# Kernel tuning notes

Measured on AMD Instinct MI355X. Metric: run time of the kernel, lower is better.

Reference implementation:

```python
import jax, jax.numpy as jnp
import numpy as np

TAU = 0.07
EPS_NORM = 1e-12  # F.normalize eps
EPS_LOG = 1e-8

N, D = 16384, 128

def setup_inputs() -> dict:
    key = jax.random.key(0)
    k1, k2, k3, k4, k5 = jax.random.split(key, 5)
    return {
        'feats': jax.random.normal(k1, (N, D), dtype=jnp.float32),
        'times': jax.random.uniform(k2, (N,), dtype=jnp.float32),
        'events': jax.random.randint(k3, (N,), 0, 2, dtype=jnp.int32),
        'ipcw_weights': jax.random.uniform(k4, (N,), dtype=jnp.float32),
        'proto': jax.random.normal(k5, (D,), dtype=jnp.float32),
    }

def _l2_normalize(x, axis):
    n = jnp.sqrt(jnp.sum(x * x, axis=axis, keepdims=True))
    return x / jnp.maximum(n, EPS_NORM)

def reference(feats, times, events, ipcw_weights, proto):
    feats_n = _l2_normalize(feats, axis=1)          # [N, D]
    proto_n = _l2_normalize(proto, axis=0)          # [D]
    logits = (feats_n @ proto_n) / TAU              # [N]
    # riskmask[i, j] = 1 if times[j] >= times[i]
    riskmask = (times[None, :] >= times[:, None]).astype(jnp.float32)  # [N, N]
    exp_logits = jnp.exp(logits)[None, :] * riskmask                    # [N, N]
    denom = exp_logits.sum(axis=1)                                      # [N]
    log_denom = jnp.log(denom + EPS_LOG)
    ev = events.astype(jnp.float32)
    loss_vec = -(logits - log_denom) * ev * ipcw_weights
    normalizer = (ev * ipcw_weights).sum()
    return loss_vec.sum() / (normalizer + EPS_LOG)
```

## Files before the change

### kernel.cpp

```cpp
#include <hip/hip_runtime.h>
#include <math.h>

#define NROWS 16384
#define DDIM  128
#define JCHUNK 2048

__device__ __forceinline__ float wave_reduce_sum(float v) {
    #pragma unroll
    for (int m = 32; m >= 1; m >>= 1) v += __shfl_xor(v, m, 64);
    return v;
}


__global__ void k_zero(float* __restrict__ denom, float* __restrict__ acc) {
    int i = blockIdx.x * blockDim.x + threadIdx.x;
    if (i < NROWS) denom[i] = 0.0f;
    if (i < 3) acc[i] = 0.0f;
}

__global__ void k_proto_norm(const float* __restrict__ proto, float* __restrict__ ws_f) {
    int lane = threadIdx.x;
    float2 p = ((const float2*)proto)[lane];
    float s = p.x * p.x + p.y * p.y;
    s = wave_reduce_sum(s);
    if (lane == 0) ws_f[2] = 1.0f / fmaxf(sqrtf(s), 1e-12f);
}

__global__ __launch_bounds__(256) void k_logits(
    const float* __restrict__ feats, const float* __restrict__ proto,
    const float* __restrict__ times, const float* __restrict__ ws_f,
    float* __restrict__ logits, float* __restrict__ te)
{
    int wave = threadIdx.x >> 6, lane = threadIdx.x & 63;
    int row = blockIdx.x * 4 + wave;
    float2 f = ((const float2*)feats)[row * 64 + lane];
    float2 p = ((const float2*)proto)[lane];
    float d  = f.x * p.x + f.y * p.y;
    float n2 = f.x * f.x + f.y * f.y;
    d  = wave_reduce_sum(d);
    n2 = wave_reduce_sum(n2);
    if (lane == 0) {
        float sp    = ws_f[2];
        float invfn = 1.0f / fmaxf(sqrtf(n2), 1e-12f);
        float logit = (d * sp * invfn) / 0.07f;
        logits[row]     = logit;
        te[2 * row]     = times[row];
        te[2 * row + 1] = expf(logit);
    }
}

__global__ __launch_bounds__(256) void k_denom(
    const float* __restrict__ times, const float* __restrict__ te,
    float* __restrict__ denom)
{
    __shared__ float4 sh[JCHUNK / 2];
    int t = threadIdx.x;
    int i = blockIdx.x * 256 + t;
    const float4* src = (const float4*)(te + (size_t)blockIdx.y * JCHUNK * 2);
    #pragma unroll
    for (int k = 0; k < 4; ++k) sh[t + 256 * k] = src[t + 256 * k];
    __syncthreads();
    float ti  = times[i];
    float acc = 0.0f;
    #pragma unroll 8
    for (int jj = 0; jj < JCHUNK / 2; ++jj) {
        float4 v = sh[jj];
        acc += (v.x >= ti) ? v.y : 0.0f;
        acc += (v.z >= ti) ? v.w : 0.0f;
    }
    atomicAdd(&denom[i], acc);
}

__global__ __launch_bounds__(256) void k_loss(
    const float* __restrict__ logits, const float* __restrict__ denom,
    const int* __restrict__ events, const float* __restrict__ w,
    float* __restrict__ acc)
{
    int i = blockIdx.x * 256 + threadIdx.x;
    float ev = (float)events[i];
    float wv = ev * w[i];
    float l  = logits[i];
    float ld = logf(denom[i] + 1e-8f);
    float loss = -(l - ld) * wv;
    loss = wave_reduce_sum(loss);
    wv   = wave_reduce_sum(wv);
    __shared__ float s1[4], s2[4];
    int wave = threadIdx.x >> 6, lane = threadIdx.x & 63;
    if (lane == 0) { s1[wave] = loss; s2[wave] = wv; }
    __syncthreads();
    if (threadIdx.x == 0) {
        atomicAdd(&acc[0], s1[0] + s1[1] + s1[2] + s1[3]);
        atomicAdd(&acc[1], s2[0] + s2[1] + s2[2] + s2[3]);
    }
}

__global__ void k_final(const float* __restrict__ acc, float* __restrict__ out) {
    out[0] = acc[0] / (acc[1] + 1e-8f);
}

extern "C" void kernel_launch(void* const* d_in, const int* in_sizes, int n_in,
                              void* d_out, int out_size, void* d_ws, size_t ws_size,
                              hipStream_t stream) {
    const float* feats  = (const float*)d_in[0];
    const float* times  = (const float*)d_in[1];
    const int*   events = (const int*)d_in[2];
    const float* w      = (const float*)d_in[3];
    const float* proto  = (const float*)d_in[4];
    float* out  = (float*)d_out;
    float* ws_f = (float*)d_ws;

    float* acc    = ws_f;
    float* logits = ws_f + 256;
    float* denom  = ws_f + 256 + NROWS;
    float* te     = ws_f + 256 + 2 * NROWS;

    k_zero<<<(NROWS + 255) / 256, 256, 0, stream>>>(denom, acc);
    k_proto_norm<<<1, 64, 0, stream>>>(proto, ws_f);
    k_logits<<<NROWS / 4, 256, 0, stream>>>(feats, proto, times, ws_f, logits, te);
    k_denom<<<dim3(NROWS / 256, NROWS / JCHUNK), 256, 0, stream>>>(times, te, denom);
    k_loss<<<NROWS / 256, 256, 0, stream>>>(logits, denom, events, w, acc);
    k_final<<<1, 1, 0, stream>>>(acc, out);
}
```

Before: 99.42 us.

## Fuse small kernels and register-block the risk-set denominator over four rows

Drops the zeroing and prototype-norm kernels: the zeroing moves into k_logits and each wave recomputes the prototype norm. The loss and final division become one single-block kernel with no global atomics. k_denom now has each thread accumulate four rows per shared-memory load, which cuts LDS traffic per comparison. JCHUNK shrinks to 512, giving 16x32 = 512 blocks versus the previous 64x8 = 512. Launch count falls from six to three, at the cost of a serial single-block reduction and more atomics per row on denom.

```diff
diff --git a/kernel.cpp b/kernel.cpp
--- a/kernel.cpp
+++ b/kernel.cpp
@@ -3,7 +3,7 @@
 
 #define NROWS 16384
 #define DDIM  128
-#define JCHUNK 2048
+#define JCHUNK 512
 
 __device__ __forceinline__ float wave_reduce_sum(float v) {
     #pragma unroll
@@ -12,37 +12,27 @@
 }
 
 
-__global__ void k_zero(float* __restrict__ denom, float* __restrict__ acc) {
-    int i = blockIdx.x * blockDim.x + threadIdx.x;
-    if (i < NROWS) denom[i] = 0.0f;
-    if (i < 3) acc[i] = 0.0f;
-}
-
-__global__ void k_proto_norm(const float* __restrict__ proto, float* __restrict__ ws_f) {
-    int lane = threadIdx.x;
-    float2 p = ((const float2*)proto)[lane];
-    float s = p.x * p.x + p.y * p.y;
-    s = wave_reduce_sum(s);
-    if (lane == 0) ws_f[2] = 1.0f / fmaxf(sqrtf(s), 1e-12f);
-}
-
 __global__ __launch_bounds__(256) void k_logits(
     const float* __restrict__ feats, const float* __restrict__ proto,
-    const float* __restrict__ times, const float* __restrict__ ws_f,
-    float* __restrict__ logits, float* __restrict__ te)
+    const float* __restrict__ times,
+    float* __restrict__ logits, float* __restrict__ te,
+    float* __restrict__ denom)
 {
+    if (blockIdx.x < 64) denom[blockIdx.x * 256 + threadIdx.x] = 0.0f;
     int wave = threadIdx.x >> 6, lane = threadIdx.x & 63;
     int row = blockIdx.x * 4 + wave;
     float2 f = ((const float2*)feats)[row * 64 + lane];
     float2 p = ((const float2*)proto)[lane];
     float d  = f.x * p.x + f.y * p.y;
     float n2 = f.x * f.x + f.y * f.y;
+    float p2 = p.x * p.x + p.y * p.y;
     d  = wave_reduce_sum(d);
     n2 = wave_reduce_sum(n2);
+    p2 = wave_reduce_sum(p2);
     if (lane == 0) {
-        float sp    = ws_f[2];
+        float invpn = 1.0f / fmaxf(sqrtf(p2), 1e-12f);
         float invfn = 1.0f / fmaxf(sqrtf(n2), 1e-12f);
-        float logit = (d * sp * invfn) / 0.07f;
+        float logit = (d * invpn * invfn) / 0.07f;
         logits[row]     = logit;
         te[2 * row]     = times[row];
         te[2 * row + 1] = expf(logit);
@@ -55,47 +45,53 @@
 {
     __shared__ float4 sh[JCHUNK / 2];
     int t = threadIdx.x;
-    int i = blockIdx.x * 256 + t;
     const float4* src = (const float4*)(te + (size_t)blockIdx.y * JCHUNK * 2);
-    #pragma unroll
-    for (int k = 0; k < 4; ++k) sh[t + 256 * k] = src[t + 256 * k];
+    sh[t] = src[t];
+    int ibase = blockIdx.x * 1024 + t;
+    float ti0 = times[ibase];
+    float ti1 = times[ibase + 256];
+    float ti2 = times[ibase + 512];
+    float ti3 = times[ibase + 768];
     __syncthreads();
-    float ti  = times[i];
-    float acc = 0.0f;
-    #pragma unroll 8
+    float a0 = 0.f, a1 = 0.f, a2 = 0.f, a3 = 0.f;
+    #pragma unroll 4
     for (int jj = 0; jj < JCHUNK / 2; ++jj) {
         float4 v = sh[jj];
-        acc += (v.x >= ti) ? v.y : 0.0f;
-        acc += (v.z >= ti) ? v.w : 0.0f;
+        a0 += (v.x >= ti0) ? v.y : 0.0f;  a0 += (v.z >= ti0) ? v.w : 0.0f;
+        a1 += (v.x >= ti1) ? v.y : 0.0f;  a1 += (v.z >= ti1) ? v.w : 0.0f;
+        a2 += (v.x >= ti2) ? v.y : 0.0f;  a2 += (v.z >= ti2) ? v.w : 0.0f;
+        a3 += (v.x >= ti3) ? v.y : 0.0f;  a3 += (v.z >= ti3) ? v.w : 0.0f;
     }
-    atomicAdd(&denom[i], acc);
+    atomicAdd(&denom[ibase],       a0);
+    atomicAdd(&denom[ibase + 256], a1);
+    atomicAdd(&denom[ibase + 512], a2);
+    atomicAdd(&denom[ibase + 768], a3);
 }
 
-__global__ __launch_bounds__(256) void k_loss(
+__global__ __launch_bounds__(1024) void k_loss_final(
     const float* __restrict__ logits, const float* __restrict__ denom,
     const int* __restrict__ events, const float* __restrict__ w,
-    float* __restrict__ acc)
+    float* __restrict__ out)
 {
-    int i = blockIdx.x * 256 + threadIdx.x;
-    float ev = (float)events[i];
-    float wv = ev * w[i];
-    float l  = logits[i];
-    float ld = logf(denom[i] + 1e-8f);
-    float loss = -(l - ld) * wv;
-    loss = wave_reduce_sum(loss);
-    wv   = wave_reduce_sum(wv);
-    __shared__ float s1[4], s2[4];
+    float ls = 0.f, wsum = 0.f;
+    for (int i = threadIdx.x; i < NROWS; i += 1024) {
+        float ev = (float)events[i];
+        float wv = ev * w[i];
+        ls   += -(logits[i] - logf(denom[i] + 1e-8f)) * wv;
+        wsum += wv;
+    }
+    ls   = wave_reduce_sum(ls);
+    wsum = wave_reduce_sum(wsum);
+    __shared__ float s1[16], s2[16];
     int wave = threadIdx.x >> 6, lane = threadIdx.x & 63;
-    if (lane == 0) { s1[wave] = loss; s2[wave] = wv; }
+    if (lane == 0) { s1[wave] = ls; s2[wave] = wsum; }
     __syncthreads();
     if (threadIdx.x == 0) {
-        atomicAdd(&acc[0], s1[0] + s1[1] + s1[2] + s1[3]);
-        atomicAdd(&acc[1], s2[0] + s2[1] + s2[2] + s2[3]);
+        float L = 0.f, W = 0.f;
+        #pragma unroll
+        for (int k = 0; k < 16; ++k) { L += s1[k]; W += s2[k]; }
+        out[0] = L / (W + 1e-8f);
     }
-}
-
-__global__ void k_final(const float* __restrict__ acc, float* __restrict__ out) {
-    out[0] = acc[0] / (acc[1] + 1e-8f);
 }
 
 extern "C" void kernel_launch(void* const* d_in, const int* in_sizes, int n_in,
@@ -109,15 +105,11 @@
     float* out  = (float*)d_out;
     float* ws_f = (float*)d_ws;
 
-    float* acc    = ws_f;
-    float* logits = ws_f + 256;
-    float* denom  = ws_f + 256 + NROWS;
-    float* te     = ws_f + 256 + 2 * NROWS;
+    float* logits = ws_f;
+    float* denom  = ws_f + NROWS;
+    float* te     = ws_f + 2 * NROWS;
 
-    k_zero<<<(NROWS + 255) / 256, 256, 0, stream>>>(denom, acc);
-    k_proto_norm<<<1, 64, 0, stream>>>(proto, ws_f);
-    k_logits<<<NROWS / 4, 256, 0, stream>>>(feats, proto, times, ws_f, logits, te);
-    k_denom<<<dim3(NROWS / 256, NROWS / JCHUNK), 256, 0, stream>>>(times, te, denom);
-    k_loss<<<NROWS / 256, 256, 0, stream>>>(logits, denom, events, w, acc);
-    k_final<<<1, 1, 0, stream>>>(acc, out);
+    k_logits<<<NROWS / 4, 256, 0, stream>>>(feats, proto, times, logits, te, denom);
+    k_denom<<<dim3(NROWS / 1024, NROWS / JCHUNK), 256, 0, stream>>>(times, te, denom);
+    k_loss_final<<<1, 1024, 0, stream>>>(logits, denom, events, w, out);
 }
```

Result: no change. 100.0 us (+0.6%).

## Replace O(N^2) risk-set sum with time-bucket suffix scan plus in-bucket scan

Applied to the files above, without the earlier changes.

Replaces the quadratic pairwise denominator with a histogram of exp(logits) over 1024 time buckets. A single-block prefix scan produces suffix sums, entries are scattered into bucket order, and each row adds only the entries in its own bucket. Proto normalisation and zeroing are folded into the logits kernel, and the final division uses a last-block ticket, which cuts the launch count. It assumes times lie in [0,1) and are roughly uniform for good load balance, the single-block scan serialises, and floating-point summation order changes.

```diff
diff --git a/kernel.cpp b/kernel.cpp
--- a/kernel.cpp
+++ b/kernel.cpp
@@ -2,8 +2,7 @@
 #include <math.h>
 
 #define NROWS 16384
-#define DDIM  128
-#define JCHUNK 2048
+#define KB 1024
 
 __device__ __forceinline__ float wave_reduce_sum(float v) {
     #pragma unroll
@@ -11,77 +10,124 @@
     return v;
 }
 
-
-__global__ void k_zero(float* __restrict__ denom, float* __restrict__ acc) {
-    int i = blockIdx.x * blockDim.x + threadIdx.x;
-    if (i < NROWS) denom[i] = 0.0f;
-    if (i < 3) acc[i] = 0.0f;
+__device__ __forceinline__ int bucket_of(float t) {
+    int b = (int)(t * (float)KB);
+    return min(max(b, 0), KB - 1);
 }
 
-__global__ void k_proto_norm(const float* __restrict__ proto, float* __restrict__ ws_f) {
-    int lane = threadIdx.x;
-    float2 p = ((const float2*)proto)[lane];
-    float s = p.x * p.x + p.y * p.y;
-    s = wave_reduce_sum(s);
-    if (lane == 0) ws_f[2] = 1.0f / fmaxf(sqrtf(s), 1e-12f);
-}
 
 __global__ __launch_bounds__(256) void k_logits(
     const float* __restrict__ feats, const float* __restrict__ proto,
-    const float* __restrict__ times, const float* __restrict__ ws_f,
-    float* __restrict__ logits, float* __restrict__ te)
+    const float* __restrict__ times,
+    float* __restrict__ logits, float* __restrict__ e_arr,
+    int* __restrict__ b_arr, float* __restrict__ acc, int* __restrict__ done)
 {
+    if (blockIdx.x == 0) {
+        if (threadIdx.x < 2) acc[threadIdx.x] = 0.0f;
+        if (threadIdx.x == 2) *done = 0;
+    }
     int wave = threadIdx.x >> 6, lane = threadIdx.x & 63;
     int row = blockIdx.x * 4 + wave;
     float2 f = ((const float2*)feats)[row * 64 + lane];
     float2 p = ((const float2*)proto)[lane];
     float d  = f.x * p.x + f.y * p.y;
     float n2 = f.x * f.x + f.y * f.y;
+    float p2 = p.x * p.x + p.y * p.y;
     d  = wave_reduce_sum(d);
     n2 = wave_reduce_sum(n2);
+    p2 = wave_reduce_sum(p2);
     if (lane == 0) {
-        float sp    = ws_f[2];
+        float invpn = 1.0f / fmaxf(sqrtf(p2), 1e-12f);
         float invfn = 1.0f / fmaxf(sqrtf(n2), 1e-12f);
-        float logit = (d * sp * invfn) / 0.07f;
-        logits[row]     = logit;
-        te[2 * row]     = times[row];
-        te[2 * row + 1] = expf(logit);
+        float logit = (d * invpn * invfn) / 0.07f;
+        logits[row] = logit;
+        e_arr[row]  = expf(logit);
+        b_arr[row]  = bucket_of(times[row]);
     }
 }
 
-__global__ __launch_bounds__(256) void k_denom(
-    const float* __restrict__ times, const float* __restrict__ te,
-    float* __restrict__ denom)
+__global__ __launch_bounds__(1024) void k_scan(
+    const int* __restrict__ b_arr, const float* __restrict__ e_arr,
+    int* __restrict__ offsets, int* __restrict__ cursor, float* __restrict__ S)
 {
-    __shared__ float4 sh[JCHUNK / 2];
+    __shared__ int   hist[KB];
+    __shared__ float es[KB];
+    __shared__ int   wbh[16];
+    __shared__ float wbe[16];
+    __shared__ float tot_sh;
     int t = threadIdx.x;
-    int i = blockIdx.x * 256 + t;
-    const float4* src = (const float4*)(te + (size_t)blockIdx.y * JCHUNK * 2);
+    hist[t] = 0; es[t] = 0.0f;
+    __syncthreads();
     #pragma unroll
-    for (int k = 0; k < 4; ++k) sh[t + 256 * k] = src[t + 256 * k];
+    for (int k = 0; k < NROWS / 1024; ++k) {
+        int r = t + k * 1024;
+        int b = b_arr[r];
+        atomicAdd(&hist[b], 1);
+        atomicAdd(&es[b], e_arr[r]);
+    }
     __syncthreads();
-    float ti  = times[i];
-    float acc = 0.0f;
-    #pragma unroll 8
-    for (int jj = 0; jj < JCHUNK / 2; ++jj) {
-        float4 v = sh[jj];
-        acc += (v.x >= ti) ? v.y : 0.0f;
-        acc += (v.z >= ti) ? v.w : 0.0f;
+    int   h = hist[t];
+    float e = es[t];
+    int   hi = h;
+    float ei = e;
+    int lane = t & 63, wid = t >> 6;
+    #pragma unroll
+    for (int d = 1; d < 64; d <<= 1) {
+        int   hu = __shfl_up(hi, d, 64);
+        float eu = __shfl_up(ei, d, 64);
+        if (lane >= d) { hi += hu; ei += eu; }
     }
-    atomicAdd(&denom[i], acc);
+    if (lane == 63) { wbh[wid] = hi; wbe[wid] = ei; }
+    __syncthreads();
+    if (t == 0) {
+        int hb = 0; float eb = 0.0f;
+        #pragma unroll
+        for (int k = 0; k < 16; ++k) {
+            int hn = wbh[k]; float en = wbe[k];
+            wbh[k] = hb; wbe[k] = eb;
+            hb += hn; eb += en;
+        }
+        tot_sh = eb;
+    }
+    __syncthreads();
+    hi += wbh[wid];
+    ei += wbe[wid];
+    offsets[t] = hi - h;
+    cursor[t]  = hi - h;
+    S[t] = tot_sh - ei;
+    if (t == KB - 1) offsets[KB] = hi;
 }
 
-__global__ __launch_bounds__(256) void k_loss(
-    const float* __restrict__ logits, const float* __restrict__ denom,
-    const int* __restrict__ events, const float* __restrict__ w,
-    float* __restrict__ acc)
+__global__ __launch_bounds__(256) void k_scatter(
+    const float* __restrict__ times, const float* __restrict__ e_arr,
+    const int* __restrict__ b_arr, int* __restrict__ cursor,
+    float2* __restrict__ ste)
+{
+    int r = blockIdx.x * 256 + threadIdx.x;
+    int b = b_arr[r];
+    int pos = atomicAdd(&cursor[b], 1);
+    ste[pos] = make_float2(times[r], e_arr[r]);
+}
+
+__global__ __launch_bounds__(256) void k_denom_loss(
+    const float* __restrict__ times, const int* __restrict__ events,
+    const float* __restrict__ w, const float* __restrict__ logits,
+    const int* __restrict__ b_arr, const int* __restrict__ offsets,
+    const float* __restrict__ S, const float2* __restrict__ ste,
+    float* __restrict__ acc, int* __restrict__ done, float* __restrict__ out)
 {
     int i = blockIdx.x * 256 + threadIdx.x;
+    float ti = times[i];
+    int b = b_arr[i];
+    float denom = S[b];
+    int p1 = offsets[b + 1];
+    for (int p = offsets[b]; p < p1; ++p) {
+        float2 v = ste[p];
+        denom += (v.x >= ti) ? v.y : 0.0f;
+    }
     float ev = (float)events[i];
     float wv = ev * w[i];
-    float l  = logits[i];
-    float ld = logf(denom[i] + 1e-8f);
-    float loss = -(l - ld) * wv;
+    float loss = -(logits[i] - logf(denom + 1e-8f)) * wv;
     loss = wave_reduce_sum(loss);
     wv   = wave_reduce_sum(wv);
     __shared__ float s1[4], s2[4];
@@ -91,11 +137,15 @@
     if (threadIdx.x == 0) {
         atomicAdd(&acc[0], s1[0] + s1[1] + s1[2] + s1[3]);
         atomicAdd(&acc[1], s2[0] + s2[1] + s2[2] + s2[3]);
+        __threadfence();
+        int ticket = atomicAdd(done, 1);
+        if (ticket == (int)gridDim.x - 1) {
+            __threadfence();
+            float L = atomicAdd(&acc[0], 0.0f);
+            float W = atomicAdd(&acc[1], 0.0f);
+            out[0] = L / (W + 1e-8f);
+        }
     }
-}
-
-__global__ void k_final(const float* __restrict__ acc, float* __restrict__ out) {
-    out[0] = acc[0] / (acc[1] + 1e-8f);
 }
 
 extern "C" void kernel_launch(void* const* d_in, const int* in_sizes, int n_in,
@@ -109,15 +159,21 @@
     float* out  = (float*)d_out;
     float* ws_f = (float*)d_ws;
 
-    float* acc    = ws_f;
-    float* logits = ws_f + 256;
-    float* denom  = ws_f + 256 + NROWS;
-    float* te     = ws_f + 256 + 2 * NROWS;
+    float*  logits  = ws_f;
+    float*  e_arr   = ws_f + NROWS;
+    int*    b_arr   = (int*)(ws_f + 2 * NROWS);
+    float2* ste     = (float2*)(ws_f + 3 * NROWS);
+    int*    offsets = (int*)(ws_f + 5 * NROWS);
+    int*    cursor  = offsets + KB + 1;
+    float*  S       = (float*)(cursor + KB);
+    float*  acc     = S + KB;
+    int*    done    = (int*)(acc + 2);
 
-    k_zero<<<(NROWS + 255) / 256, 256, 0, stream>>>(denom, acc);
-    k_proto_norm<<<1, 64, 0, stream>>>(proto, ws_f);
-    k_logits<<<NROWS / 4, 256, 0, stream>>>(feats, proto, times, ws_f, logits, te);
-    k_denom<<<dim3(NROWS / 256, NROWS / JCHUNK), 256, 0, stream>>>(times, te, denom);
-    k_loss<<<NROWS / 256, 256, 0, stream>>>(logits, denom, events, w, acc);
-    k_final<<<1, 1, 0, stream>>>(acc, out);
+    k_logits<<<NROWS / 4, 256, 0, stream>>>(feats, proto, times,
+                                            logits, e_arr, b_arr, acc, done);
+    k_scan<<<1, 1024, 0, stream>>>(b_arr, e_arr, offsets, cursor, S);
+    k_scatter<<<NROWS / 256, 256, 0, stream>>>(times, e_arr, b_arr, cursor, ste);
+    k_denom_loss<<<NROWS / 256, 256, 0, stream>>>(times, events, w, logits,
+                                                  b_arr, offsets, S, ste,
+                                                  acc, done, out);
 }
```

Measured after the change: 108.2 us. 8.8% more time.
